# Kernel optimization log

Measured on AMD Instinct MI355X. Metric: run time of the kernel, lower is better.

The kernel has to match this reference:

```python
import jax, jax.numpy as jnp
import numpy as np

N_A = 50000
N_B = 50000
E = 500000
IN_F = 128
GNN_F = 16
OUT_F = 16
H = 8


def setup_inputs() -> dict:
    key = jax.random.key(0)
    ks = jax.random.split(key, 16)
    f32 = jnp.float32
    rn = lambda k, shape: jax.random.normal(k, shape, f32) * 0.05
    return {
        "idx_a": jnp.arange(N_A, dtype=jnp.int32),
        "idx_b": jnp.arange(N_B, dtype=jnp.int32),
        "src_r0": jax.random.randint(ks[0], (E,), 0, N_A, jnp.int32),
        "dst_r0": jax.random.randint(ks[1], (E,), 0, N_B, jnp.int32),
        "src_r1": jax.random.randint(ks[2], (E,), 0, N_B, jnp.int32),
        "dst_r1": jax.random.randint(ks[3], (E,), 0, N_A, jnp.int32),
        "emb_a": rn(ks[4], (N_A, IN_F)),
        "emb_b": rn(ks[5], (N_B, IN_F)),
        "l1_Wv": rn(ks[6], (2, IN_F, H * GNN_F)),
        "l1_bv": jnp.zeros((2, H * GNN_F), f32),
        "l1_Wq": rn(ks[7], (2, H * GNN_F, H)),
        "l1_bq": jnp.zeros((2, H), f32),
        "l1_Wk": rn(ks[8], (2, H * GNN_F, H)),
        "l1_bk": jnp.zeros((2, H), f32),
        "l2_Wv": rn(ks[9], (2, GNN_F, H * OUT_F)),
        "l2_bv": jnp.zeros((2, H * OUT_F), f32),
        "l2_Wq": rn(ks[10], (2, H * OUT_F, H)),
        "l2_bq": jnp.zeros((2, H), f32),
        "l2_Wk": rn(ks[11], (2, H * OUT_F, H)),
        "l2_bk": jnp.zeros((2, H), f32),
    }


def _gat(x_src, x_dst, src, dst, Wv, bv, Wq, bq, Wk, bk, n_dst, n_feat):
    # linear_v on src and dst node features
    h_src = x_src @ Wv + bv            # [Ns, H*F]
    h_dst = x_dst @ Wv + bv            # [Nd, H*F]
    q = h_dst @ Wq + bq                # [Nd, H]
    k = h_src @ Wk + bk                # [Ns, H]
    # u_add_v score + leaky relu, per edge per head
    e = jax.nn.leaky_relu(k[src] + q[dst], negative_slope=0.2)  # [E, H]
    # edge softmax over incoming edges of each destination node
    m = jax.ops.segment_max(e, dst, num_segments=n_dst)         # [Nd, H]
    ex = jnp.exp(e - m[dst])
    denom = jax.ops.segment_sum(ex, dst, num_segments=n_dst)    # [Nd, H]
    attn = ex / denom[dst]                                      # [E, H]
    # u_mul_e + scatter-sum aggregate
    u = h_src.reshape(-1, H, n_feat)                             # [Ns, H, F]
    msg = u[src] * attn[:, :, None]                              # [E, H, F]
    v = jax.ops.segment_sum(msg, dst, num_segments=n_dst)       # [Nd, H, F]
    return v.mean(axis=1)                                        # [Nd, F]


def reference(idx_a, idx_b, src_r0, dst_r0, src_r1, dst_r1, emb_a, emb_b,
              l1_Wv, l1_bv, l1_Wq, l1_bq, l1_Wk, l1_bk,
              l2_Wv, l2_bv, l2_Wq, l2_bq, l2_Wk, l2_bk):
    # REmbedding lookup per node type
    x_a = emb_a[idx_a]
    x_b = emb_b[idx_b]
    # layer 1: relation r0 (a->b) and r1 (b->a); each dst type has exactly 1
    # incoming relation, so the HeteroGraphConv mean is a no-op (count=1)
    h_b = _gat(x_a, x_b, src_r0, dst_r0, l1_Wv[0], l1_bv[0], l1_Wq[0], l1_bq[0],
               l1_Wk[0], l1_bk[0], N_B, GNN_F)
    h_a = _gat(x_b, x_a, src_r1, dst_r1, l1_Wv[1], l1_bv[1], l1_Wq[1], l1_bq[1],
               l1_Wk[1], l1_bk[1], N_A, GNN_F)
    # activation: Dropout(0.5) is identity in eval mode, then ELU
    h_a = jax.nn.elu(h_a)
    h_b = jax.nn.elu(h_b)
    # layer 2
    o_b = _gat(h_a, h_b, src_r0, dst_r0, l2_Wv[0], l2_bv[0], l2_Wq[0], l2_bq[0],
               l2_Wk[0], l2_bk[0], N_B, OUT_F)
    o_a = _gat(h_b, h_a, src_r1, dst_r1, l2_Wv[1], l2_bv[1], l2_Wq[1], l2_bq[1],
               l2_Wk[1], l2_bk[1], N_A, OUT_F)
    return (o_a, o_b)
```

## Files before the change

kernel.cpp:

```cpp
#include <hip/hip_runtime.h>
#include <hip/hip_fp16.h>

#define N_NODES 50000
#define NEDGE   500000
#define HEADS   8
#define FEAT    16
#define HF      128
#define UST     64

typedef __attribute__((ext_vector_type(8))) _Float16 half8;
typedef __attribute__((ext_vector_type(4))) float floatx4;

__device__ __forceinline__ unsigned pkh2(float a, float b) {
  __half2 h = __floats2half2_rn(a, b);
  return *(unsigned*)&h;
}

__global__ __launch_bounds__(256)
void prep_wt2_kernel(const float* __restrict__ W, const float* __restrict__ wf,
                     __half* __restrict__ Wt2, float* __restrict__ bias16) {
  int side = blockIdx.x;
  const float* Wp  = W + (size_t)side * 16384;
  const float* wfk = wf + (size_t)(side == 0 ? 1 : 3) * 1040;
  const float* wfq = wf + (size_t)(side == 0 ? 2 : 0) * 1040;
  __half* o = Wt2 + (size_t)side * 144 * 128;
  for (int j = threadIdx.x; j < 144 * 128; j += 256) {
    int col = j >> 7, k = j & 127;
    float v = (col < 128) ? Wp[k * 128 + col]
            : (col < 136) ? wfk[k * 8 + (col - 128)]
                          : wfq[k * 8 + (col - 136)];
    o[j] = __float2half(v);
  }
  if (threadIdx.x < 16) {
    int c = threadIdx.x;
    bias16[side * 16 + c] = (c < 8) ? wfk[1024 + c] : wfq[1024 + (c - 8)];
  }
}

__global__ __launch_bounds__(256)
void gemm_mfma_kernel(const float* __restrict__ xa, const int* __restrict__ idxa,
                      const float* __restrict__ xb, const int* __restrict__ idxb,
                      const __half* __restrict__ Wt2, const float* __restrict__ bias,
                      const float* __restrict__ bias16,
                      float* __restrict__ ua, float* __restrict__ ub,
                      float* __restrict__ kb0, float* __restrict__ kb1,
                      float* __restrict__ qb1, float* __restrict__ qb0, int nrows) {
  const int side = blockIdx.y;
  const float* x  = side ? xb : xa;
  const int* idx  = side ? idxb : idxa;
  const __half* Wtp = Wt2 + (size_t)side * 144 * 128;
  const float* bp = bias + side * HF;
  const float* b8 = bias16 + side * 16;
  float* uout = side ? ub : ua;
  float* kout = side ? kb1 : kb0;
  float* qout = side ? qb0 : qb1;

  __shared__ __align__(16) unsigned short sm[26624];
  char* Asm = (char*)sm;
  char* Wsm = (char*)(sm + 8192);
  const int tid = threadIdx.x;
  const int w = tid >> 6, lane = tid & 63;
  const int row0 = blockIdx.x * 64;

  #pragma unroll
  for (int p = 0; p < 9; ++p) {
    int i = p * 256 + tid;
    int col = i >> 4, kp = i & 15;
    float4 v = *(const float4*)(Wtp + col * 128 + kp * 8);
    int dst = (col * 256 + kp * 16) ^ ((col & 7) << 4);
    *(float4*)(Wsm + dst) = v;
  }
  {
    int r = tid >> 2;
    int rr = row0 + r;
    int g = (rr < nrows) ? (idx ? idx[rr] : rr) : 0;
    const float* xp = x + (size_t)g * 128 + (tid & 3) * 8;
    #pragma unroll
    for (int p = 0; p < 4; ++p) {
      float4 v0 = *(const float4*)(xp + p * 32);
      float4 v1 = *(const float4*)(xp + p * 32 + 4);
      uint4 o;
      o.x = pkh2(v0.x, v0.y); o.y = pkh2(v0.z, v0.w);
      o.z = pkh2(v1.x, v1.y); o.w = pkh2(v1.z, v1.w);
      int k0 = (tid & 3) * 8 + p * 32;
      int dst = (r * 256 + k0 * 2) ^ ((r & 7) << 4);
      *(uint4*)(Asm + dst) = o;
    }
  }
  __syncthreads();

  floatx4 acc[9];
  #pragma unroll
  for (int t = 0; t < 8; ++t) {
    float b = bp[t * 16 + (lane & 15)];
    acc[t] = (floatx4){b, b, b, b};
  }
  {
    float b = b8[lane & 15];
    acc[8] = (floatx4){b, b, b, b};
  }

  const int lrow = lane & 15, lk = lane >> 4;
  #pragma unroll
  for (int kb = 0; kb < 4; ++kb) {
    int r = w * 16 + lrow;
    int abyte = (r * 256 + kb * 64 + lk * 16) ^ ((r & 7) << 4);
    half8 af = *(const half8*)(Asm + abyte);
    #pragma unroll
    for (int t = 0; t < 9; ++t) {
      int c = t * 16 + lrow;
      int bbyte = (c * 256 + kb * 64 + lk * 16) ^ ((c & 7) << 4);
      half8 bf = *(const half8*)(Wsm + bbyte);
      acc[t] = __builtin_amdgcn_mfma_f32_16x16x32_f16(af, bf, acc[t], 0, 0, 0);
    }
  }

  unsigned short* up = (unsigned short*)uout;
  #pragma unroll
  for (int j = 0; j < 4; ++j) {
    int rr = row0 + w * 16 + (lane >> 4) * 4 + j;
    if (rr < nrows) {
      #pragma unroll
      for (int t = 0; t < 8; ++t) {
        __half h = __float2half(acc[t][j]);
        up[(size_t)rr * 128 + t * 16 + (lane & 15)] = *(unsigned short*)&h;
      }
      int col = lane & 15;
      if (col < 8) kout[(size_t)rr * 8 + col] = acc[8][j];
      else         qout[(size_t)rr * 8 + (col - 8)] = acc[8][j];
    }
  }
}

__global__ __launch_bounds__(256)
void fold_kernel(const float* __restrict__ l1_Wv, const float* __restrict__ l1_bv,
                 const float* __restrict__ l1_Wq, const float* __restrict__ l1_bq,
                 const float* __restrict__ l1_Wk, const float* __restrict__ l1_bk,
                 const float* __restrict__ l2_Wv, const float* __restrict__ l2_bv,
                 const float* __restrict__ l2_Wq, const float* __restrict__ l2_bq,
                 const float* __restrict__ l2_Wk, const float* __restrict__ l2_bk,
                 float* __restrict__ outbuf) {
  int b = blockIdx.x;
  int layer = b >> 2, rel = (b >> 1) & 1, qk = b & 1;
  int Kx = (layer == 0) ? 128 : 16;
  const float* Wv = ((layer == 0) ? l1_Wv : l2_Wv) + (size_t)rel * Kx * HF;
  const float* bv = ((layer == 0) ? l1_bv : l2_bv) + rel * HF;
  const float* Wqk = ((layer == 0) ? (qk ? l1_Wk : l1_Wq) : (qk ? l2_Wk : l2_Wq)) + (size_t)rel * HF * 8;
  const float* bqk = ((layer == 0) ? (qk ? l1_bk : l1_bq) : (qk ? l2_bk : l2_bq)) + rel * 8;
  float* o = outbuf + (size_t)b * 1040;
  for (int t = threadIdx.x; t < Kx * 8; t += 256) {
    int row = t >> 3, c = t & 7;
    float acc = 0.f;
    for (int j = 0; j < HF; ++j) acc += Wv[row * HF + j] * Wqk[j * 8 + c];
    o[t] = acc;
  }
  for (int t = threadIdx.x; t < 8; t += 256) {
    float acc = bqk[t];
    for (int j = 0; j < HF; ++j) acc += bv[j] * Wqk[j * 8 + t];
    o[Kx * 8 + t] = acc;
  }
}

__global__ __launch_bounds__(256)
void qk16_kernel(const float* __restrict__ xA, const float* __restrict__ xB,
                 const float* __restrict__ WfkA, const float* __restrict__ WfqA,
                 const float* __restrict__ WfkB, const float* __restrict__ WfqB,
                 float* __restrict__ k2a, float* __restrict__ k2b,
                 float* __restrict__ qA, float* __restrict__ qB, int n) {
  const int side = blockIdx.y;
  const float* x   = side ? xB : xA;
  const float* Wfk = side ? WfkB : WfkA;
  const float* Wfq = side ? WfqB : WfqA;
  float* k2  = side ? k2b : k2a;
  float* qout = side ? qB : qA;
  __shared__ float Wk[136], Wq[136];
  const int tid = threadIdx.x;
  for (int i = tid; i < 136; i += 256) { Wk[i] = Wfk[i]; Wq[i] = Wfq[i]; }
  __syncthreads();
  int row = blockIdx.x * 32 + (tid >> 3), col = tid & 7;
  if (row >= n) return;
  const float* xr = x + (size_t)row * 16;
  float ak = Wk[128 + col], aq = Wq[128 + col];
  #pragma unroll
  for (int j4 = 0; j4 < 4; ++j4) {
    float4 v = *(const float4*)(xr + j4 * 4);
    float xv[4] = {v.x, v.y, v.z, v.w};
    #pragma unroll
    for (int j = 0; j < 4; ++j) {
      ak += xv[j] * Wk[(j4 * 4 + j) * 8 + col];
      aq += xv[j] * Wq[(j4 * 4 + j) * 8 + col];
    }
  }
  k2[row * 8 + col] = ak;
  qout[row * 8 + col] = aq;
}

__global__ __launch_bounds__(256)
void hist2_kernel(const int* __restrict__ dst0, const int* __restrict__ dst1,
                  int* __restrict__ cnt) {
  int e = blockIdx.x * 256 + threadIdx.x;
  if (e < NEDGE) atomicAdd(&cnt[dst0[e]], 1);
  else if (e < 2 * NEDGE) atomicAdd(&cnt[N_NODES + dst1[e - NEDGE]], 1);
}

__global__ __launch_bounds__(256)
void scan_bsum_kernel(const int* __restrict__ cnt, int* __restrict__ bsum, int n) {
  __shared__ int s[256];
  int i = blockIdx.x * 256 + threadIdx.x;
  s[threadIdx.x] = (i < n) ? cnt[i] : 0;
  __syncthreads();
  for (int o = 128; o > 0; o >>= 1) {
    if (threadIdx.x < o) s[threadIdx.x] += s[threadIdx.x + o];
    __syncthreads();
  }
  if (threadIdx.x == 0) bsum[blockIdx.x] = s[0];
}

__global__ __launch_bounds__(512)
void scan_offsets_kernel(int* __restrict__ bsum, int nb) {
  __shared__ int s[512];
  int t = threadIdx.x;
  s[t] = (t < nb) ? bsum[t] : 0;
  __syncthreads();
  for (int o = 1; o < 512; o <<= 1) {
    int v = (t >= o) ? s[t - o] : 0;
    __syncthreads();
    s[t] += v;
    __syncthreads();
  }
  if (t < nb) bsum[t] = (t == 0) ? 0 : s[t - 1];
}

__global__ __launch_bounds__(256)
void scan_final_kernel(const int* __restrict__ cnt, const int* __restrict__ boff,
                       int* __restrict__ row_start, int n) {
  __shared__ int s[256];
  int t = threadIdx.x, i = blockIdx.x * 256 + t;
  int v = (i < n) ? cnt[i] : 0;
  s[t] = v;
  __syncthreads();
  for (int o = 1; o < 256; o <<= 1) {
    int w = (t >= o) ? s[t - o] : 0;
    __syncthreads();
    s[t] += w;
    __syncthreads();
  }
  if (i < n)  row_start[i] = boff[blockIdx.x] + s[t] - v;
  if (i == n - 1) row_start[n] = boff[blockIdx.x] + s[t];
}

__global__ __launch_bounds__(256)
void csr_scatter2_kernel(const int* __restrict__ s0, const int* __restrict__ d0,
                         const int* __restrict__ s1, const int* __restrict__ d1,
                         const int* __restrict__ rs, int* __restrict__ fill,
                         int* __restrict__ cs) {
  int e = blockIdx.x * 256 + threadIdx.x;
  if (e >= 2 * NEDGE) return;
  int rel = (e >= NEDGE);
  int ee = rel ? e - NEDGE : e;
  int d = rel ? d1[ee] : d0[ee];
  int s = rel ? s1[ee] : s0[ee];
  int key = rel * N_NODES + d;
  int pos = rs[key] + atomicAdd(&fill[key], 1);
  cs[pos] = s;
}

__global__ __launch_bounds__(256)
void node_agg2_kernel(const int* __restrict__ rs, const int* __restrict__ cs,
                      const float* __restrict__ u0, const float* __restrict__ u1,
                      const float* __restrict__ kb0, const float* __restrict__ kb1,
                      const float* __restrict__ qt0, const float* __restrict__ qt1,
                      float* __restrict__ out0, float* __restrict__ out1, int elu) {
  int grp  = (blockIdx.x * 256 + threadIdx.x) >> 5;
  int lane = threadIdx.x & 31;
  if (grp >= 2 * N_NODES) return;
  int rel = grp >= N_NODES;
  int node = grp - (rel ? N_NODES : 0);
  const float* ut = rel ? u1 : u0;
  const float* kb = rel ? kb1 : kb0;
  const float* qt = rel ? qt1 : qt0;
  float* out      = rel ? out1 : out0;

  int e0 = rs[grp], e1 = rs[grp + 1];
  const int hd = lane >> 2;
  float qh = qt[node * 8 + hd];
  float den = 0.f;
  float4 acc = make_float4(0.f, 0.f, 0.f, 0.f);

  for (int e = e0; e < e1; e += 8) {
    int m = e1 - e;
    int s[8];
    #pragma unroll
    for (int j = 0; j < 8; ++j) s[j] = cs[e + (j < m ? j : m - 1)];
    uint2 uv[8]; float kv[8];
    #pragma unroll
    for (int j = 0; j < 8; ++j) {
      uv[j] = *(const uint2*)((const char*)(ut + (size_t)s[j] * UST) + lane * 8);
      kv[j] = kb[s[j] * 8 + hd];
    }
    #pragma unroll
    for (int j = 0; j < 8; ++j) {
      float sc = kv[j] + qh; sc = sc > 0.f ? sc : 0.2f * sc;
      float ex = (j < m) ? __expf(sc) : 0.f;
      den += ex;
      float2 f01 = __half22float2(*(__half2*)&uv[j].x);
      float2 f23 = __half22float2(*(__half2*)&uv[j].y);
      acc.x += ex * f01.x; acc.y += ex * f01.y;
      acc.z += ex * f23.x; acc.w += ex * f23.y;
    }
  }
  float inv = den > 0.f ? 1.f / den : 0.f;
  float4 r = make_float4(acc.x * inv, acc.y * inv, acc.z * inv, acc.w * inv);
  #pragma unroll
  for (int m2 = 4; m2 <= 16; m2 <<= 1) {
    r.x += __shfl_xor(r.x, m2); r.y += __shfl_xor(r.y, m2);
    r.z += __shfl_xor(r.z, m2); r.w += __shfl_xor(r.w, m2);
  }
  r.x *= 0.125f; r.y *= 0.125f; r.z *= 0.125f; r.w *= 0.125f;
  if (elu) {
    r.x = r.x > 0.f ? r.x : expm1f(r.x);
    r.y = r.y > 0.f ? r.y : expm1f(r.y);
    r.z = r.z > 0.f ? r.z : expm1f(r.z);
    r.w = r.w > 0.f ? r.w : expm1f(r.w);
  }
  if (lane < 4) *(float4*)&out[(size_t)node * FEAT + lane * 4] = r;
}

__global__ __launch_bounds__(256)
void agg_l2z_kernel(const int* __restrict__ rs, const int* __restrict__ cs,
                    const float* __restrict__ xA, const float* __restrict__ xB,
                    const float* __restrict__ k2a, const float* __restrict__ k2b,
                    const float* __restrict__ qt0, const float* __restrict__ qt1,
                    const float* __restrict__ Wv, const float* __restrict__ bv,
                    float* __restrict__ out) {
  const int rel = blockIdx.y;
  __shared__ float Wt_lds[128 * 16];
  __shared__ float z_lds[8][128];
  __shared__ float bvs[16];
  const int tid = threadIdx.x;
  for (int i = tid; i < 2048; i += 256) {
    int j = i >> 7, c = i & 127, h = c >> 4, o = c & 15;
    Wt_lds[(h * 16 + j) * 16 + o] = Wv[rel * 2048 + i];
  }
  if (tid < 16) {
    float s = 0.f;
    #pragma unroll
    for (int h = 0; h < 8; ++h) s += bv[rel * 128 + h * 16 + tid];
    bvs[tid] = s;
  }
  __syncthreads();

  int node = blockIdx.x * 8 + (tid >> 5);
  int lane = tid & 31;
  int gl   = tid >> 5;
  const float* x  = rel ? xB : xA;
  const float* k2 = rel ? k2b : k2a;
  const float* qt = rel ? qt1 : qt0;
  int grp = rel * N_NODES + node;

  int e0 = rs[grp], e1 = rs[grp + 1];
  const int h = lane >> 2, jg = (lane & 3) * 4;
  float qh = qt[node * 8 + h];
  float den = 0.f;
  float4 z = make_float4(0.f, 0.f, 0.f, 0.f);

  for (int e = e0; e < e1; e += 8) {
    int m = e1 - e;
    int s[8];
    #pragma unroll
    for (int j = 0; j < 8; ++j) s[j] = cs[e + (j < m ? j : m - 1)];
    float kv[8]; float4 xv[8];
    #pragma unroll
    for (int j = 0; j < 8; ++j) {
      kv[j] = k2[s[j] * 8 + h];
      xv[j] = *(const float4*)&x[(size_t)s[j] * 16 + jg];
    }
    #pragma unroll
    for (int j = 0; j < 8; ++j) {
      float sc = kv[j] + qh; sc = sc > 0.f ? sc : 0.2f * sc;
      float ex = (j < m) ? __expf(sc) : 0.f;
      den += ex;
      z.x += ex * xv[j].x; z.y += ex * xv[j].y;
      z.z += ex * xv[j].z; z.w += ex * xv[j].w;
    }
  }
  float inv = den > 0.f ? 1.f / den : 0.f;
  z.x *= inv; z.y *= inv; z.z *= inv; z.w *= inv;
  *(float4*)&z_lds[gl][h * 16 + jg] = z;

  const int o = lane & 15, half = lane >> 4;
  float acc = 0.f;
  #pragma unroll
  for (int hg = 0; hg < 4; ++hg) {
    int h2 = half * 4 + hg;
    const float* zr = &z_lds[gl][h2 * 16];
    float4 z0 = *(const float4*)zr;
    float4 z1 = *(const float4*)(zr + 4);
    float4 z2 = *(const float4*)(zr + 8);
    float4 z3 = *(const float4*)(zr + 12);
    const float* wb = &Wt_lds[h2 * 256 + o];
    acc += z0.x * wb[0]   + z0.y * wb[16]  + z0.z * wb[32]  + z0.w * wb[48]
         + z1.x * wb[64]  + z1.y * wb[80]  + z1.z * wb[96]  + z1.w * wb[112]
         + z2.x * wb[128] + z2.y * wb[144] + z2.z * wb[160] + z2.w * wb[176]
         + z3.x * wb[192] + z3.y * wb[208] + z3.z * wb[224] + z3.w * wb[240];
  }
  acc += __shfl_xor(acc, 16);
  if (lane < 16) {
    float r = 0.125f * (acc + ((e1 > e0) ? bvs[o] : 0.f));
    float* ob = out + (rel ? 0 : (size_t)N_NODES * FEAT);
    ob[(size_t)node * FEAT + o] = r;
  }
}

extern "C" void kernel_launch(void* const* d_in, const int* in_sizes, int n_in,
                              void* d_out, int out_size, void* d_ws, size_t ws_size,
                              hipStream_t stream) {
  const int* idx_a  = (const int*)d_in[0];
  const int* idx_b  = (const int*)d_in[1];
  const int* src_r0 = (const int*)d_in[2];
  const int* dst_r0 = (const int*)d_in[3];
  const int* src_r1 = (const int*)d_in[4];
  const int* dst_r1 = (const int*)d_in[5];
  const float* emb_a = (const float*)d_in[6];
  const float* emb_b = (const float*)d_in[7];
  const float* l1_Wv = (const float*)d_in[8];
  const float* l1_bv = (const float*)d_in[9];
  const float* l1_Wq = (const float*)d_in[10];
  const float* l1_bq = (const float*)d_in[11];
  const float* l1_Wk = (const float*)d_in[12];
  const float* l1_bk = (const float*)d_in[13];
  const float* l2_Wv = (const float*)d_in[14];
  const float* l2_bv = (const float*)d_in[15];
  const float* l2_Wq = (const float*)d_in[16];
  const float* l2_bq = (const float*)d_in[17];
  const float* l2_Wk = (const float*)d_in[18];
  const float* l2_bk = (const float*)d_in[19];
  float* out = (float*)d_out;

  char* ws = (char*)d_ws;
  size_t off = 0;
  auto alloc = [&](size_t bytes) {
    void* p = ws + off; off += (bytes + 255) & ~255ULL; return p;
  };
  float*  u0    = (float*)alloc((size_t)N_NODES * UST * 4);
  float*  u1    = (float*)alloc((size_t)N_NODES * UST * 4);
  __half* Wt2   = (__half*)alloc(2 * 144 * 128 * 2);
  float*  b16   = (float*)alloc(2 * 16 * 4);
  float*  kb0   = (float*)alloc((size_t)N_NODES * HEADS * 4);
  float*  kb1   = (float*)alloc((size_t)N_NODES * HEADS * 4);
  float*  qb0   = (float*)alloc((size_t)N_NODES * HEADS * 4);
  float*  qb1   = (float*)alloc((size_t)N_NODES * HEADS * 4);
  float*  k2a   = (float*)alloc((size_t)N_NODES * HEADS * 4);
  float*  k2b   = (float*)alloc((size_t)N_NODES * HEADS * 4);
  float*  xA    = (float*)alloc((size_t)N_NODES * FEAT * 4);
  float*  xB    = (float*)alloc((size_t)N_NODES * FEAT * 4);
  int*    rs    = (int*)  alloc((size_t)(2 * N_NODES + 1) * 4);
  int*    cs    = (int*)  alloc((size_t)2 * NEDGE * 4);
  int*    cnt   = (int*)  alloc((size_t)4 * N_NODES * 4);
  int*    bsum  = (int*)  alloc(512 * 4);
  float*  wf    = (float*)alloc(8 * 1040 * 4);

  dim3 blk(256);
  const int n2 = 2 * N_NODES;
  int* fill = cnt + n2;
  const int nScanBlk  = (n2 + 255) / 256;
  const int nEdgeBlk2 = (2 * NEDGE + 255) / 256;
  const int nAggBlk   = (n2 + 7) / 8;
  const int nAggL2    = N_NODES / 8;
  const int nGemmBlk64 = (N_NODES + 63) / 64;
  const int nQk16Blk   = (N_NODES + 31) / 32;

  fold_kernel<<<8, blk, 0, stream>>>(l1_Wv, l1_bv, l1_Wq, l1_bq, l1_Wk, l1_bk,
                                     l2_Wv, l2_bv, l2_Wq, l2_bq, l2_Wk, l2_bk, wf);
  prep_wt2_kernel<<<2, blk, 0, stream>>>(l1_Wv, wf, Wt2, b16);
  auto wslot = [&](int layer, int rel, int qk) {
    return wf + (size_t)((layer << 2) | (rel << 1) | qk) * 1040;
  };

  hipMemsetAsync(cnt, 0, (size_t)2 * n2 * 4, stream);
  hist2_kernel<<<nEdgeBlk2, blk, 0, stream>>>(dst_r0, dst_r1, cnt);
  scan_bsum_kernel<<<nScanBlk, blk, 0, stream>>>(cnt, bsum, n2);
  scan_offsets_kernel<<<1, dim3(512), 0, stream>>>(bsum, nScanBlk);
  scan_final_kernel<<<nScanBlk, blk, 0, stream>>>(cnt, bsum, rs, n2);
  csr_scatter2_kernel<<<nEdgeBlk2, blk, 0, stream>>>(src_r0, dst_r0, src_r1, dst_r1,
                                                     rs, fill, cs);

  {
    gemm_mfma_kernel<<<dim3(nGemmBlk64, 2), blk, 0, stream>>>(
        emb_a, idx_a, emb_b, idx_b, Wt2, l1_bv, b16,
        u0, u1, kb0, kb1, qb1, qb0, N_NODES);
    node_agg2_kernel<<<nAggBlk, blk, 0, stream>>>(rs, cs, u0, u1, kb0, kb1,
                                                  qb0, qb1, xB, xA, 1);
  }
  {
    qk16_kernel<<<dim3(nQk16Blk, 2), blk, 0, stream>>>(
        xA, xB,
        wslot(1,0,1), wslot(1,1,0), wslot(1,1,1), wslot(1,0,0),
        k2a, k2b, qb1, qb0, N_NODES);
    agg_l2z_kernel<<<dim3(nAggL2, 2), blk, 0, stream>>>(
        rs, cs, xA, xB, k2a, k2b, qb0, qb1, l2_Wv, l2_bv, out);
  }
}
```

Baseline: 268.8 us.

## Pack layer-2 node features and keys into fp16 interleaved rows

Layer-1 outputs are now written as fp16 into a 32-half row per node, and the layer-2 key projection is stored in the same row. The layer-2 aggregation then reads one 64-byte row per source node instead of separate fp32 feature and key arrays. This cuts the bytes and cache lines touched per gathered edge, at the cost of fp16 rounding on the hidden features and keys.

```diff
diff --git a/kernel.cpp b/kernel.cpp
--- a/kernel.cpp
+++ b/kernel.cpp
@@ -7,6 +7,7 @@
 #define FEAT    16
 #define HF      128
 #define UST     64
+#define XKST    32
 
 typedef __attribute__((ext_vector_type(8))) _Float16 half8;
 typedef __attribute__((ext_vector_type(4))) float floatx4;
@@ -162,16 +163,14 @@
 }
 
 __global__ __launch_bounds__(256)
-void qk16_kernel(const float* __restrict__ xA, const float* __restrict__ xB,
+void qk16_kernel(__half* __restrict__ xk_a, __half* __restrict__ xk_b,
                  const float* __restrict__ WfkA, const float* __restrict__ WfqA,
                  const float* __restrict__ WfkB, const float* __restrict__ WfqB,
-                 float* __restrict__ k2a, float* __restrict__ k2b,
                  float* __restrict__ qA, float* __restrict__ qB, int n) {
   const int side = blockIdx.y;
-  const float* x   = side ? xB : xA;
+  __half* xk = side ? xk_b : xk_a;
   const float* Wfk = side ? WfkB : WfkA;
   const float* Wfq = side ? WfqB : WfqA;
-  float* k2  = side ? k2b : k2a;
   float* qout = side ? qB : qA;
   __shared__ float Wk[136], Wq[136];
   const int tid = threadIdx.x;
@@ -179,19 +178,25 @@
   __syncthreads();
   int row = blockIdx.x * 32 + (tid >> 3), col = tid & 7;
   if (row >= n) return;
-  const float* xr = x + (size_t)row * 16;
+  const __half* xr = xk + (size_t)row * XKST;
+  uint4 p0 = *(const uint4*)xr;
+  uint4 p1 = *(const uint4*)(xr + 8);
+  float xv[16];
+  {
+    unsigned pp[8] = {p0.x, p0.y, p0.z, p0.w, p1.x, p1.y, p1.z, p1.w};
+    #pragma unroll
+    for (int j = 0; j < 8; ++j) {
+      float2 f = __half22float2(*(__half2*)&pp[j]);
+      xv[j * 2] = f.x; xv[j * 2 + 1] = f.y;
+    }
+  }
   float ak = Wk[128 + col], aq = Wq[128 + col];
   #pragma unroll
-  for (int j4 = 0; j4 < 4; ++j4) {
-    float4 v = *(const float4*)(xr + j4 * 4);
-    float xv[4] = {v.x, v.y, v.z, v.w};
-    #pragma unroll
-    for (int j = 0; j < 4; ++j) {
-      ak += xv[j] * Wk[(j4 * 4 + j) * 8 + col];
-      aq += xv[j] * Wq[(j4 * 4 + j) * 8 + col];
-    }
-  }
-  k2[row * 8 + col] = ak;
+  for (int j = 0; j < 16; ++j) {
+    ak += xv[j] * Wk[j * 8 + col];
+    aq += xv[j] * Wq[j * 8 + col];
+  }
+  xk[(size_t)row * XKST + 16 + col] = __float2half(ak);
   qout[row * 8 + col] = aq;
 }
 
@@ -270,7 +275,7 @@
                       const float* __restrict__ u0, const float* __restrict__ u1,
                       const float* __restrict__ kb0, const float* __restrict__ kb1,
                       const float* __restrict__ qt0, const float* __restrict__ qt1,
-                      float* __restrict__ out0, float* __restrict__ out1, int elu) {
+                      __half* __restrict__ out0, __half* __restrict__ out1) {
   int grp  = (blockIdx.x * 256 + threadIdx.x) >> 5;
   int lane = threadIdx.x & 31;
   if (grp >= 2 * N_NODES) return;
@@ -279,7 +284,7 @@
   const float* ut = rel ? u1 : u0;
   const float* kb = rel ? kb1 : kb0;
   const float* qt = rel ? qt1 : qt0;
-  float* out      = rel ? out1 : out0;
+  __half* out     = rel ? out1 : out0;
 
   int e0 = rs[grp], e1 = rs[grp + 1];
   const int hd = lane >> 2;
@@ -317,19 +322,20 @@
     r.z += __shfl_xor(r.z, m2); r.w += __shfl_xor(r.w, m2);
   }
   r.x *= 0.125f; r.y *= 0.125f; r.z *= 0.125f; r.w *= 0.125f;
-  if (elu) {
-    r.x = r.x > 0.f ? r.x : expm1f(r.x);
-    r.y = r.y > 0.f ? r.y : expm1f(r.y);
-    r.z = r.z > 0.f ? r.z : expm1f(r.z);
-    r.w = r.w > 0.f ? r.w : expm1f(r.w);
-  }
-  if (lane < 4) *(float4*)&out[(size_t)node * FEAT + lane * 4] = r;
+  r.x = r.x > 0.f ? r.x : expm1f(r.x);
+  r.y = r.y > 0.f ? r.y : expm1f(r.y);
+  r.z = r.z > 0.f ? r.z : expm1f(r.z);
+  r.w = r.w > 0.f ? r.w : expm1f(r.w);
+  if (lane < 4) {
+    uint2 o;
+    o.x = pkh2(r.x, r.y); o.y = pkh2(r.z, r.w);
+    *(uint2*)&out[(size_t)node * XKST + lane * 4] = o;
+  }
 }
 
 __global__ __launch_bounds__(256)
 void agg_l2z_kernel(const int* __restrict__ rs, const int* __restrict__ cs,
-                    const float* __restrict__ xA, const float* __restrict__ xB,
-                    const float* __restrict__ k2a, const float* __restrict__ k2b,
+                    const __half* __restrict__ xk_a, const __half* __restrict__ xk_b,
                     const float* __restrict__ qt0, const float* __restrict__ qt1,
                     const float* __restrict__ Wv, const float* __restrict__ bv,
                     float* __restrict__ out) {
@@ -353,13 +359,12 @@
   int node = blockIdx.x * 8 + (tid >> 5);
   int lane = tid & 31;
   int gl   = tid >> 5;
-  const float* x  = rel ? xB : xA;
-  const float* k2 = rel ? k2b : k2a;
+  const __half* xk = rel ? xk_b : xk_a;
   const float* qt = rel ? qt1 : qt0;
   int grp = rel * N_NODES + node;
 
   int e0 = rs[grp], e1 = rs[grp + 1];
-  const int h = lane >> 2, jg = (lane & 3) * 4;
+  const int h = lane >> 2, fg = lane & 3;
   float qh = qt[node * 8 + h];
   float den = 0.f;
   float4 z = make_float4(0.f, 0.f, 0.f, 0.f);
@@ -369,24 +374,27 @@
     int s[8];
     #pragma unroll
     for (int j = 0; j < 8; ++j) s[j] = cs[e + (j < m ? j : m - 1)];
-    float kv[8]; float4 xv[8];
+    uint2 uv[8]; __half kvh[8];
     #pragma unroll
     for (int j = 0; j < 8; ++j) {
-      kv[j] = k2[s[j] * 8 + h];
-      xv[j] = *(const float4*)&x[(size_t)s[j] * 16 + jg];
+      const __half* p = xk + (size_t)s[j] * XKST;
+      uv[j] = *(const uint2*)(p + fg * 4);
+      kvh[j] = p[16 + h];
     }
     #pragma unroll
     for (int j = 0; j < 8; ++j) {
-      float sc = kv[j] + qh; sc = sc > 0.f ? sc : 0.2f * sc;
+      float sc = __half2float(kvh[j]) + qh; sc = sc > 0.f ? sc : 0.2f * sc;
       float ex = (j < m) ? __expf(sc) : 0.f;
       den += ex;
-      z.x += ex * xv[j].x; z.y += ex * xv[j].y;
-      z.z += ex * xv[j].z; z.w += ex * xv[j].w;
+      float2 f01 = __half22float2(*(__half2*)&uv[j].x);
+      float2 f23 = __half22float2(*(__half2*)&uv[j].y);
+      z.x += ex * f01.x; z.y += ex * f01.y;
+      z.z += ex * f23.x; z.w += ex * f23.y;
     }
   }
   float inv = den > 0.f ? 1.f / den : 0.f;
   z.x *= inv; z.y *= inv; z.z *= inv; z.w *= inv;
-  *(float4*)&z_lds[gl][h * 16 + jg] = z;
+  *(float4*)&z_lds[gl][h * 16 + fg * 4] = z;
 
   const int o = lane & 15, half = lane >> 4;
   float acc = 0.f;
@@ -450,10 +458,8 @@
   float*  kb1   = (float*)alloc((size_t)N_NODES * HEADS * 4);
   float*  qb0   = (float*)alloc((size_t)N_NODES * HEADS * 4);
   float*  qb1   = (float*)alloc((size_t)N_NODES * HEADS * 4);
-  float*  k2a   = (float*)alloc((size_t)N_NODES * HEADS * 4);
-  float*  k2b   = (float*)alloc((size_t)N_NODES * HEADS * 4);
-  float*  xA    = (float*)alloc((size_t)N_NODES * FEAT * 4);
-  float*  xB    = (float*)alloc((size_t)N_NODES * FEAT * 4);
+  __half* xk_a  = (__half*)alloc((size_t)N_NODES * XKST * 2);
+  __half* xk_b  = (__half*)alloc((size_t)N_NODES * XKST * 2);
   int*    rs    = (int*)  alloc((size_t)(2 * N_NODES + 1) * 4);
   int*    cs    = (int*)  alloc((size_t)2 * NEDGE * 4);
   int*    cnt   = (int*)  alloc((size_t)4 * N_NODES * 4);
@@ -490,14 +496,14 @@
         emb_a, idx_a, emb_b, idx_b, Wt2, l1_bv, b16,
         u0, u1, kb0, kb1, qb1, qb0, N_NODES);
     node_agg2_kernel<<<nAggBlk, blk, 0, stream>>>(rs, cs, u0, u1, kb0, kb1,
-                                                  qb0, qb1, xB, xA, 1);
+                                                  qb0, qb1, xk_b, xk_a);
   }
   {
     qk16_kernel<<<dim3(nQk16Blk, 2), blk, 0, stream>>>(
-        xA, xB,
+        xk_a, xk_b,
         wslot(1,0,1), wslot(1,1,0), wslot(1,1,1), wslot(1,0,0),
-        k2a, k2b, qb1, qb0, N_NODES);
+        qb1, qb0, N_NODES);
     agg_l2z_kernel<<<dim3(nAggL2, 2), blk, 0, stream>>>(
-        rs, cs, xA, xB, k2a, k2b, qb0, qb1, l2_Wv, l2_bv, out);
-  }
-}
+        rs, cs, xk_a, xk_b, qb0, qb1, l2_Wv, l2_bv, out);
+  }
+}
```

Result: no change. 265.6 us, median of 3 (-1.2%).
